# Optimization experiments

Measured on AMD Instinct MI355X. Metric: run time of the kernel, lower is better.

## Reference

```python
import jax, jax.numpy as jnp
import numpy as np

N_NODES = 50000
N_EDGES = 640000
N_REL = 200
D_IN = 128
D_OUT = 128


def setup_inputs() -> dict:
    key = jax.random.key(0)
    k1, k2, k3, k4, k5, k6 = jax.random.split(key, 6)
    x = jax.random.normal(k1, (N_NODES, D_IN), dtype=jnp.float32)
    edge_index = jax.random.randint(k2, (2, N_EDGES), 0, N_NODES, dtype=jnp.int64)
    edge_type = jax.random.randint(k3, (N_EDGES,), 0, N_REL, dtype=jnp.int64)
    rel_emb = jax.random.normal(k4, (N_REL, D_IN), dtype=jnp.float32)
    # nn.Linear weights stored as [out_features, in_features]
    W_lin = jax.random.normal(k5, (D_OUT, D_IN), dtype=jnp.float32) * (1.0 / np.sqrt(D_IN))
    # xavier_uniform for attn kernel [1, D_IN]
    limit = np.sqrt(6.0 / (1 + D_IN))
    W_attn = jax.random.uniform(k6, (1, D_IN), dtype=jnp.float32, minval=-limit, maxval=limit)
    return {"x": x, "edge_index": edge_index, "edge_type": edge_type,
            "rel_emb": rel_emb, "W_lin": W_lin, "W_attn": W_attn}


def reference(x, edge_index, edge_type, rel_emb, W_lin, W_attn):
    # x: [N, D_in]; edge_index: [2, E]; edge_type: [E]; rel_emb: [R, D_in]
    x_trans = x @ W_lin.T                       # [N, D_out]
    src_idx, tgt_idx = edge_index[0], edge_index[1]
    h_src = x[src_idx]                          # [E, D_in] gather
    h_rel = rel_emb[edge_type]                  # [E, D_in] gather
    sum_feat = h_src + h_rel                    # [E, D_in]
    attn = jax.nn.sigmoid(sum_feat @ W_attn.T)  # [E, 1]
    msg = x_trans[src_idx] * attn               # [E, D_out]
    out = jax.ops.segment_sum(msg, tgt_idx, num_segments=x.shape[0])  # [N, D_out]
    return jax.nn.relu(out)
```

## Files before the change

### kernel.cpp

```cpp
#include <hip/hip_runtime.h>
#include <hip/hip_bf16.h>

#define N_NODES 50000
#define N_EDGES 640000
#define N_REL   200
#define D       128
#define CAP     64
#define RANGES  8
#define NODES_PER_RANGE (N_NODES / RANGES)
#define CHUNK_EDGES 2560
#define N_CHUNKS (N_EDGES / CHUNK_EDGES)

typedef __attribute__((ext_vector_type(8))) short short8;
typedef __attribute__((ext_vector_type(4))) float floatx4;
typedef __attribute__((ext_vector_type(4))) unsigned uintx4;

__device__ __forceinline__ unsigned short f2bf(float f) {
    unsigned u = __float_as_uint(f);
    u += 0x7FFF + ((u >> 16) & 1);
    return (unsigned short)(u >> 16);
}

__device__ __forceinline__ float sigmoidf(float x) {
    return 1.f / (1.f + __expf(-x));
}

__global__ __launch_bounds__(256) void setup_kernel(
        const float* __restrict__ W,
        const float* __restrict__ rel,
        const float* __restrict__ Wattn,
        unsigned short* __restrict__ Wbf,
        float* __restrict__ s_rel,
        int* __restrict__ count) {
    const int b = blockIdx.x;
    if (b < 64) {
        const int i = b * 256 + threadIdx.x;
        Wbf[i] = f2bf(W[i]);
    } else if (b < 114) {
        const int wave = (b - 64) * 4 + (threadIdx.x >> 6);
        const int lane = threadIdx.x & 63;
        if (wave < N_REL) {
            const float* __restrict__ row = rel + (size_t)wave * D;
            float a = fmaf(row[lane], Wattn[lane],
                           row[lane + 64] * Wattn[lane + 64]);
#pragma unroll
            for (int off = 32; off; off >>= 1)
                a += __shfl_down(a, off);
            if (lane == 0) s_rel[wave] = a;
        }
    } else {
        const int i = (b - 114) * 256 + threadIdx.x;
        if (i < N_NODES) count[i] = 0;
    }
}

__global__ __launch_bounds__(256) void xtrans_mfma_kernel(
        const float* __restrict__ x,
        const unsigned short* __restrict__ Wbf,
        const float* __restrict__ Wattn,
        unsigned short* __restrict__ xt,
        float* __restrict__ s_node) {
    const int wid = (blockIdx.x * blockDim.x + threadIdx.x) >> 6;
    if (wid >= N_NODES / 16) return;
    const int lane = threadIdx.x & 63;
    const int r16  = lane & 15;
    const int quad = lane >> 4;
    const int m0   = wid * 16;

    short8 af[4];
    float  sn = 0.f;
#pragma unroll
    for (int s = 0; s < 4; ++s) {
        const int k0 = s * 32 + quad * 8;
        const float* __restrict__ xr = x + (size_t)(m0 + r16) * D + k0;
        const float4 lo = *(const float4*)(xr);
        const float4 hi = *(const float4*)(xr + 4);
        const float4 wl = *(const float4*)(Wattn + k0);
        const float4 wh = *(const float4*)(Wattn + k0 + 4);
        sn = fmaf(lo.x, wl.x, sn); sn = fmaf(lo.y, wl.y, sn);
        sn = fmaf(lo.z, wl.z, sn); sn = fmaf(lo.w, wl.w, sn);
        sn = fmaf(hi.x, wh.x, sn); sn = fmaf(hi.y, wh.y, sn);
        sn = fmaf(hi.z, wh.z, sn); sn = fmaf(hi.w, wh.w, sn);
        short8 a;
        a[0] = (short)f2bf(lo.x); a[1] = (short)f2bf(lo.y);
        a[2] = (short)f2bf(lo.z); a[3] = (short)f2bf(lo.w);
        a[4] = (short)f2bf(hi.x); a[5] = (short)f2bf(hi.y);
        a[6] = (short)f2bf(hi.z); a[7] = (short)f2bf(hi.w);
        af[s] = a;
    }
    sn += __shfl_xor(sn, 16);
    sn += __shfl_xor(sn, 32);
    if (lane < 16) s_node[m0 + r16] = sn;

#pragma unroll
    for (int t = 0; t < 8; ++t) {
        floatx4 acc = {0.f, 0.f, 0.f, 0.f};
#pragma unroll
        for (int s = 0; s < 4; ++s) {
            const int k0 = s * 32 + quad * 8;
            const short8 b = *(const short8*)(Wbf + (size_t)(t * 16 + r16) * D + k0);
            acc = __builtin_amdgcn_mfma_f32_16x16x32_bf16(af[s], b, acc, 0, 0, 0);
        }
#pragma unroll
        for (int r = 0; r < 4; ++r) {
            const int orow = m0 + quad * 4 + r;
            xt[(size_t)orow * D + t * 16 + r16] = f2bf(acc[r]);
        }
    }
}

__global__ __launch_bounds__(256) void scatter_kernel(
        const int* __restrict__ src_idx,
        const int* __restrict__ tgt_idx,
        const int* __restrict__ etype,
        const float* __restrict__ s_node,
        const float* __restrict__ s_rel,
        int* __restrict__ count,
        unsigned* __restrict__ sorted) {
    __shared__ float ls_rel[N_REL];
    if (threadIdx.x < N_REL) ls_rel[threadIdx.x] = s_rel[threadIdx.x];
    __syncthreads();

    const int b     = blockIdx.x;
    const int lo    = (b & 7) * NODES_PER_RANGE;
    const int hi    = lo + NODES_PER_RANGE;
    const int base  = (b >> 3) * CHUNK_EDGES + threadIdx.x;

#pragma unroll
    for (int it = 0; it < CHUNK_EDGES / 256; ++it) {
        const int e = base + it * 256;
        const int t = tgt_idx[e];
        const int s = src_idx[e];
        const int r = etype[e];
        if (t >= lo && t < hi) {
            const float logit = s_node[s] + ls_rel[r];
            const unsigned rec =
                ((unsigned)f2bf(sigmoidf(logit)) << 16) | (unsigned)s;
            const int k = atomicAdd(&count[t], 1);
            sorted[t * CAP + k] = rec;
        }
    }
}

__device__ __forceinline__ void gproc(unsigned r, const unsigned short* __restrict__ xt,
                                      int sub, floatx4& acc) {
    const unsigned src = r & 0xFFFFu;
    const float a = __uint_as_float(r & 0xFFFF0000u);
    const uint2 p = *(const uint2*)(xt + (size_t)src * D + sub * 4);
    acc[0] = fmaf(a, __uint_as_float(p.x << 16),         acc[0]);
    acc[1] = fmaf(a, __uint_as_float(p.x & 0xFFFF0000u), acc[1]);
    acc[2] = fmaf(a, __uint_as_float(p.y << 16),         acc[2]);
    acc[3] = fmaf(a, __uint_as_float(p.y & 0xFFFF0000u), acc[3]);
}

__global__ __launch_bounds__(256) void gather_kernel(
        const int* __restrict__ count,
        const unsigned* __restrict__ sorted,
        const unsigned short* __restrict__ xt,
        float* __restrict__ out) {
    const int wid  = (blockIdx.x * blockDim.x + threadIdx.x) >> 6;
    const int lane = threadIdx.x & 63;
    const int half = lane >> 5;
    const int sub  = lane & 31;
    const int t    = wid * 2 + half;
    if (t >= N_NODES) return;

    const int cnt = count[t];
    const unsigned* __restrict__ rec = sorted + (size_t)t * CAP;

    floatx4 acc = {0.f, 0.f, 0.f, 0.f};
    int i = 0;
    for (; i + 4 <= cnt; i += 4) {
        const uintx4 r4 = __builtin_nontemporal_load((const uintx4*)(rec + i));
        gproc(r4.x, xt, sub, acc);
        gproc(r4.y, xt, sub, acc);
        gproc(r4.z, xt, sub, acc);
        gproc(r4.w, xt, sub, acc);
    }
    for (; i < cnt; ++i)
        gproc(__builtin_nontemporal_load(rec + i), xt, sub, acc);

    floatx4 o;
    o[0] = fmaxf(acc[0], 0.f);
    o[1] = fmaxf(acc[1], 0.f);
    o[2] = fmaxf(acc[2], 0.f);
    o[3] = fmaxf(acc[3], 0.f);
    __builtin_nontemporal_store(o, (floatx4*)(out + (size_t)t * D) + sub);
}

extern "C" void kernel_launch(void* const* d_in, const int* in_sizes, int n_in,
                              void* d_out, int out_size, void* d_ws, size_t ws_size,
                              hipStream_t stream) {
    const float* x        = (const float*)d_in[0];
    const int*   edge_idx = (const int*)d_in[1];
    const int*   etype    = (const int*)d_in[2];
    const float* rel_emb  = (const float*)d_in[3];
    const float* W_lin    = (const float*)d_in[4];
    const float* W_attn   = (const float*)d_in[5];
    float* out = (float*)d_out;

    const int* src_idx = edge_idx;
    const int* tgt_idx = edge_idx + N_EDGES;

    unsigned short* xt   = (unsigned short*)d_ws;
    float* s_node        = (float*)(xt + (size_t)N_NODES * D);
    float* s_rel         = s_node + N_NODES;
    unsigned short* Wbf  = (unsigned short*)(s_rel + N_REL);
    int*   count         = (int*)(Wbf + D * D);
    unsigned* sorted     = (unsigned*)(count + N_NODES);

    setup_kernel<<<dim3(310), dim3(256), 0, stream>>>(
        W_lin, rel_emb, W_attn, Wbf, s_rel, count);

    xtrans_mfma_kernel<<<dim3((N_NODES / 16 * 64 + 255) / 256), dim3(256), 0, stream>>>(
        x, Wbf, W_attn, xt, s_node);

    scatter_kernel<<<dim3(N_CHUNKS * RANGES), dim3(256), 0, stream>>>(
        src_idx, tgt_idx, etype, s_node, s_rel, count, sorted);

    gather_kernel<<<dim3(N_NODES / 8), dim3(256), 0, stream>>>(
        count, sorted, xt, out);
}
```

Before: 168.1 us.

## Fuse setup and xtrans into one kernel with LDS-staged bf16 weights; widen gather

Merges the weight-conversion setup kernel and the MFMA projection kernel into one launch. Each projection block converts W to bf16 into swizzled shared memory and reads MFMA B fragments from LDS instead of a global bf16 copy. The gather kernel now gives each node 16 lanes, each loading 8 bf16 values, and interleaves blocks across the 8 node ranges to match the scatter partitioning. This saves one launch and gives wider per-lane loads, but every block now converts the full weight matrix redundantly and uses 32KB of LDS, which may lower occupancy.

Result: faster. 155.5 us (-7.5%).

```diff
diff --git a/kernel.cpp b/kernel.cpp
--- a/kernel.cpp
+++ b/kernel.cpp
@@ -11,6 +11,14 @@
 #define CHUNK_EDGES 2560
 #define N_CHUNKS (N_EDGES / CHUNK_EDGES)
 
+#define XT_WAVES   (N_NODES / 16)
+#define XT_BLOCKS  782
+#define SREL_BLOCKS 50
+#define CNT_BLOCKS 196
+#define PRE_BLOCKS (XT_BLOCKS + SREL_BLOCKS + CNT_BLOCKS)
+
+#define G_BLOCKS_PER_RANGE 391
+
 typedef __attribute__((ext_vector_type(8))) short short8;
 typedef __attribute__((ext_vector_type(4))) float floatx4;
 typedef __attribute__((ext_vector_type(4))) unsigned uintx4;
@@ -25,19 +33,88 @@
     return 1.f / (1.f + __expf(-x));
 }
 
-__global__ __launch_bounds__(256) void setup_kernel(
+__global__ __launch_bounds__(256) void pre_kernel(
+        const float* __restrict__ x,
         const float* __restrict__ W,
         const float* __restrict__ rel,
         const float* __restrict__ Wattn,
-        unsigned short* __restrict__ Wbf,
+        unsigned short* __restrict__ xt,
+        float* __restrict__ s_node,
         float* __restrict__ s_rel,
         int* __restrict__ count) {
+    __shared__ unsigned short lw[D * D];
     const int b = blockIdx.x;
-    if (b < 64) {
-        const int i = b * 256 + threadIdx.x;
-        Wbf[i] = f2bf(W[i]);
-    } else if (b < 114) {
-        const int wave = (b - 64) * 4 + (threadIdx.x >> 6);
+
+    if (b < XT_BLOCKS) {
+        const int tid = threadIdx.x;
+#pragma unroll
+        for (int i = 0; i < 8; ++i) {
+            const int idx8 = tid + i * 256;
+            const int row  = idx8 >> 4;
+            const int kk   = idx8 & 15;
+            const float* __restrict__ wr = W + (size_t)row * D + kk * 8;
+            const float4 lo = *(const float4*)(wr);
+            const float4 hi = *(const float4*)(wr + 4);
+            short8 v;
+            v[0] = (short)f2bf(lo.x); v[1] = (short)f2bf(lo.y);
+            v[2] = (short)f2bf(lo.z); v[3] = (short)f2bf(lo.w);
+            v[4] = (short)f2bf(hi.x); v[5] = (short)f2bf(hi.y);
+            v[6] = (short)f2bf(hi.z); v[7] = (short)f2bf(hi.w);
+            const int slot = (row * 16 + kk) ^ (row & 7);
+            *(short8*)((char*)lw + slot * 16) = v;
+        }
+        __syncthreads();
+
+        const int wid = b * 4 + (threadIdx.x >> 6);
+        if (wid >= XT_WAVES) return;
+        const int lane = threadIdx.x & 63;
+        const int r16  = lane & 15;
+        const int quad = lane >> 4;
+        const int m0   = wid * 16;
+
+        short8 af[4];
+        float  sn = 0.f;
+#pragma unroll
+        for (int s = 0; s < 4; ++s) {
+            const int k0 = s * 32 + quad * 8;
+            const float* __restrict__ xr = x + (size_t)(m0 + r16) * D + k0;
+            const float4 lo = *(const float4*)(xr);
+            const float4 hi = *(const float4*)(xr + 4);
+            const float4 wl = *(const float4*)(Wattn + k0);
+            const float4 wh = *(const float4*)(Wattn + k0 + 4);
+            sn = fmaf(lo.x, wl.x, sn); sn = fmaf(lo.y, wl.y, sn);
+            sn = fmaf(lo.z, wl.z, sn); sn = fmaf(lo.w, wl.w, sn);
+            sn = fmaf(hi.x, wh.x, sn); sn = fmaf(hi.y, wh.y, sn);
+            sn = fmaf(hi.z, wh.z, sn); sn = fmaf(hi.w, wh.w, sn);
+            short8 a;
+            a[0] = (short)f2bf(lo.x); a[1] = (short)f2bf(lo.y);
+            a[2] = (short)f2bf(lo.z); a[3] = (short)f2bf(lo.w);
+            a[4] = (short)f2bf(hi.x); a[5] = (short)f2bf(hi.y);
+            a[6] = (short)f2bf(hi.z); a[7] = (short)f2bf(hi.w);
+            af[s] = a;
+        }
+        sn += __shfl_xor(sn, 16);
+        sn += __shfl_xor(sn, 32);
+        if (lane < 16) s_node[m0 + r16] = sn;
+
+#pragma unroll
+        for (int t = 0; t < 8; ++t) {
+            floatx4 acc = {0.f, 0.f, 0.f, 0.f};
+            const int row = t * 16 + r16;
+#pragma unroll
+            for (int s = 0; s < 4; ++s) {
+                const int slot = (row * 16 + s * 4 + quad) ^ (row & 7);
+                const short8 bfrag = *(const short8*)((const char*)lw + slot * 16);
+                acc = __builtin_amdgcn_mfma_f32_16x16x32_bf16(af[s], bfrag, acc, 0, 0, 0);
+            }
+#pragma unroll
+            for (int r = 0; r < 4; ++r) {
+                const int orow = m0 + quad * 4 + r;
+                xt[(size_t)orow * D + t * 16 + r16] = f2bf(acc[r]);
+            }
+        }
+    } else if (b < XT_BLOCKS + SREL_BLOCKS) {
+        const int wave = (b - XT_BLOCKS) * 4 + (threadIdx.x >> 6);
         const int lane = threadIdx.x & 63;
         if (wave < N_REL) {
             const float* __restrict__ row = rel + (size_t)wave * D;
@@ -49,63 +126,8 @@
             if (lane == 0) s_rel[wave] = a;
         }
     } else {
-        const int i = (b - 114) * 256 + threadIdx.x;
+        const int i = (b - XT_BLOCKS - SREL_BLOCKS) * 256 + threadIdx.x;
         if (i < N_NODES) count[i] = 0;
-    }
-}
-
-__global__ __launch_bounds__(256) void xtrans_mfma_kernel(
-        const float* __restrict__ x,
-        const unsigned short* __restrict__ Wbf,
-        const float* __restrict__ Wattn,
-        unsigned short* __restrict__ xt,
-        float* __restrict__ s_node) {
-    const int wid = (blockIdx.x * blockDim.x + threadIdx.x) >> 6;
-    if (wid >= N_NODES / 16) return;
-    const int lane = threadIdx.x & 63;
-    const int r16  = lane & 15;
-    const int quad = lane >> 4;
-    const int m0   = wid * 16;
-
-    short8 af[4];
-    float  sn = 0.f;
-#pragma unroll
-    for (int s = 0; s < 4; ++s) {
-        const int k0 = s * 32 + quad * 8;
-        const float* __restrict__ xr = x + (size_t)(m0 + r16) * D + k0;
-        const float4 lo = *(const float4*)(xr);
-        const float4 hi = *(const float4*)(xr + 4);
-        const float4 wl = *(const float4*)(Wattn + k0);
-        const float4 wh = *(const float4*)(Wattn + k0 + 4);
-        sn = fmaf(lo.x, wl.x, sn); sn = fmaf(lo.y, wl.y, sn);
-        sn = fmaf(lo.z, wl.z, sn); sn = fmaf(lo.w, wl.w, sn);
-        sn = fmaf(hi.x, wh.x, sn); sn = fmaf(hi.y, wh.y, sn);
-        sn = fmaf(hi.z, wh.z, sn); sn = fmaf(hi.w, wh.w, sn);
-        short8 a;
-        a[0] = (short)f2bf(lo.x); a[1] = (short)f2bf(lo.y);
-        a[2] = (short)f2bf(lo.z); a[3] = (short)f2bf(lo.w);
-        a[4] = (short)f2bf(hi.x); a[5] = (short)f2bf(hi.y);
-        a[6] = (short)f2bf(hi.z); a[7] = (short)f2bf(hi.w);
-        af[s] = a;
-    }
-    sn += __shfl_xor(sn, 16);
-    sn += __shfl_xor(sn, 32);
-    if (lane < 16) s_node[m0 + r16] = sn;
-
-#pragma unroll
-    for (int t = 0; t < 8; ++t) {
-        floatx4 acc = {0.f, 0.f, 0.f, 0.f};
-#pragma unroll
-        for (int s = 0; s < 4; ++s) {
-            const int k0 = s * 32 + quad * 8;
-            const short8 b = *(const short8*)(Wbf + (size_t)(t * 16 + r16) * D + k0);
-            acc = __builtin_amdgcn_mfma_f32_16x16x32_bf16(af[s], b, acc, 0, 0, 0);
-        }
-#pragma unroll
-        for (int r = 0; r < 4; ++r) {
-            const int orow = m0 + quad * 4 + r;
-            xt[(size_t)orow * D + t * 16 + r16] = f2bf(acc[r]);
-        }
     }
 }
 
@@ -142,15 +164,19 @@
     }
 }
 
-__device__ __forceinline__ void gproc(unsigned r, const unsigned short* __restrict__ xt,
-                                      int sub, floatx4& acc) {
+__device__ __forceinline__ void gproc4(unsigned r, const unsigned short* __restrict__ xt,
+                                       int sub, floatx4& a0, floatx4& a1) {
     const unsigned src = r & 0xFFFFu;
     const float a = __uint_as_float(r & 0xFFFF0000u);
-    const uint2 p = *(const uint2*)(xt + (size_t)src * D + sub * 4);
-    acc[0] = fmaf(a, __uint_as_float(p.x << 16),         acc[0]);
-    acc[1] = fmaf(a, __uint_as_float(p.x & 0xFFFF0000u), acc[1]);
-    acc[2] = fmaf(a, __uint_as_float(p.y << 16),         acc[2]);
-    acc[3] = fmaf(a, __uint_as_float(p.y & 0xFFFF0000u), acc[3]);
+    const uint4 p = *(const uint4*)(xt + (size_t)src * D + sub * 8);
+    a0[0] = fmaf(a, __uint_as_float(p.x << 16),         a0[0]);
+    a0[1] = fmaf(a, __uint_as_float(p.x & 0xFFFF0000u), a0[1]);
+    a0[2] = fmaf(a, __uint_as_float(p.y << 16),         a0[2]);
+    a0[3] = fmaf(a, __uint_as_float(p.y & 0xFFFF0000u), a0[3]);
+    a1[0] = fmaf(a, __uint_as_float(p.z << 16),         a1[0]);
+    a1[1] = fmaf(a, __uint_as_float(p.z & 0xFFFF0000u), a1[1]);
+    a1[2] = fmaf(a, __uint_as_float(p.w << 16),         a1[2]);
+    a1[3] = fmaf(a, __uint_as_float(p.w & 0xFFFF0000u), a1[3]);
 }
 
 __global__ __launch_bounds__(256) void gather_kernel(
@@ -158,34 +184,40 @@
         const unsigned* __restrict__ sorted,
         const unsigned short* __restrict__ xt,
         float* __restrict__ out) {
-    const int wid  = (blockIdx.x * blockDim.x + threadIdx.x) >> 6;
-    const int lane = threadIdx.x & 63;
-    const int half = lane >> 5;
-    const int sub  = lane & 31;
-    const int t    = wid * 2 + half;
-    if (t >= N_NODES) return;
+    const int rng   = blockIdx.x & 7;
+    const int idx   = blockIdx.x >> 3;
+    const int w     = threadIdx.x >> 6;
+    const int lane  = threadIdx.x & 63;
+    const int q     = lane >> 4;
+    const int sub   = lane & 15;
+    const int local = idx * 16 + w * 4 + q;
+    if (local >= NODES_PER_RANGE) return;
+    const int t = rng * NODES_PER_RANGE + local;
 
     const int cnt = count[t];
     const unsigned* __restrict__ rec = sorted + (size_t)t * CAP;
 
-    floatx4 acc = {0.f, 0.f, 0.f, 0.f};
+    floatx4 a0 = {0.f, 0.f, 0.f, 0.f};
+    floatx4 a1 = {0.f, 0.f, 0.f, 0.f};
     int i = 0;
     for (; i + 4 <= cnt; i += 4) {
         const uintx4 r4 = __builtin_nontemporal_load((const uintx4*)(rec + i));
-        gproc(r4.x, xt, sub, acc);
-        gproc(r4.y, xt, sub, acc);
-        gproc(r4.z, xt, sub, acc);
-        gproc(r4.w, xt, sub, acc);
+        gproc4(r4.x, xt, sub, a0, a1);
+        gproc4(r4.y, xt, sub, a0, a1);
+        gproc4(r4.z, xt, sub, a0, a1);
+        gproc4(r4.w, xt, sub, a0, a1);
     }
     for (; i < cnt; ++i)
-        gproc(__builtin_nontemporal_load(rec + i), xt, sub, acc);
-
-    floatx4 o;
-    o[0] = fmaxf(acc[0], 0.f);
-    o[1] = fmaxf(acc[1], 0.f);
-    o[2] = fmaxf(acc[2], 0.f);
-    o[3] = fmaxf(acc[3], 0.f);
-    __builtin_nontemporal_store(o, (floatx4*)(out + (size_t)t * D) + sub);
+        gproc4(__builtin_nontemporal_load(rec + i), xt, sub, a0, a1);
+
+    floatx4 o0, o1;
+    o0[0] = fmaxf(a0[0], 0.f); o0[1] = fmaxf(a0[1], 0.f);
+    o0[2] = fmaxf(a0[2], 0.f); o0[3] = fmaxf(a0[3], 0.f);
+    o1[0] = fmaxf(a1[0], 0.f); o1[1] = fmaxf(a1[1], 0.f);
+    o1[2] = fmaxf(a1[2], 0.f); o1[3] = fmaxf(a1[3], 0.f);
+    floatx4* orow = (floatx4*)(out + (size_t)t * D) + sub * 2;
+    __builtin_nontemporal_store(o0, orow);
+    __builtin_nontemporal_store(o1, orow + 1);
 }
 
 extern "C" void kernel_launch(void* const* d_in, const int* in_sizes, int n_in,
@@ -205,19 +237,15 @@
     unsigned short* xt   = (unsigned short*)d_ws;
     float* s_node        = (float*)(xt + (size_t)N_NODES * D);
     float* s_rel         = s_node + N_NODES;
-    unsigned short* Wbf  = (unsigned short*)(s_rel + N_REL);
-    int*   count         = (int*)(Wbf + D * D);
+    int*   count         = (int*)(s_rel + N_REL);
     unsigned* sorted     = (unsigned*)(count + N_NODES);
 
-    setup_kernel<<<dim3(310), dim3(256), 0, stream>>>(
-        W_lin, rel_emb, W_attn, Wbf, s_rel, count);
-
-    xtrans_mfma_kernel<<<dim3((N_NODES / 16 * 64 + 255) / 256), dim3(256), 0, stream>>>(
-        x, Wbf, W_attn, xt, s_node);
+    pre_kernel<<<dim3(PRE_BLOCKS), dim3(256), 0, stream>>>(
+        x, W_lin, rel_emb, W_attn, xt, s_node, s_rel, count);
 
     scatter_kernel<<<dim3(N_CHUNKS * RANGES), dim3(256), 0, stream>>>(
         src_idx, tgt_idx, etype, s_node, s_rel, count, sorted);
 
-    gather_kernel<<<dim3(N_NODES / 8), dim3(256), 0, stream>>>(
+    gather_kernel<<<dim3(G_BLOCKS_PER_RANGE * RANGES), dim3(256), 0, stream>>>(
         count, sorted, xt, out);
 }
```
